# Kernel optimization log

Hardware: AMD Instinct MI355X
Metric: run time of the kernel (lower is better)

## Reference

```python
import jax, jax.numpy as jnp
import numpy as np

# ---- architecture constants (from init_kwargs) ----
BIG_K, SMALL_K = 51, 5
C_OUT, GROUP_IN = 96, 4
NK = -(-BIG_K // SMALL_K)          # 11 small kernels tile the big kernel
C_IN = C_OUT * NK                  # 1056
PADDING = SMALL_K - 1              # 4
EXTRA_PAD = PADDING - SMALL_K // 2 # 2
MID = BIG_K // 2                   # 25
REAL_PAD = [MID - i * SMALL_K - PADDING for i in range(NK)]
B, HOUT, WOUT = 8, 56, 56
HIN = HOUT + 2 * EXTRA_PAD         # 60


def setup_inputs() -> dict:
    key = jax.random.key(0)
    k1, k2, k3, k4 = jax.random.split(key, 4)
    rng = np.random.default_rng(0)
    rp = np.asarray(REAL_PAD, dtype=np.int32)
    # pad_hv: (C_IN, 2*GROUP_IN). Columns 0..G-1 horizontal shifts, G..2G-1 vertical.
    # For each (output-channel block, column) the nk channels get a random permutation of REAL_PAD.
    pad_hv = np.empty((C_IN, 2 * GROUP_IN), dtype=np.int32)
    for g in range(2 * GROUP_IN):
        for co in range(C_OUT):
            pad_hv[co * NK:(co + 1) * NK, g] = rng.permutation(rp)
    # idx_identit: (C_OUT, GROUP_IN); one randomly chosen channel inside each block.
    idx_identit = (rng.integers(0, NK, size=(C_OUT, GROUP_IN)) + np.arange(C_OUT)[:, None] * NK).astype(np.int32)
    x = jax.random.normal(k1, (B, C_IN, HIN, HIN), dtype=jnp.float32)
    w1 = jax.random.uniform(k2, (C_IN * GROUP_IN,), dtype=jnp.float32)
    w2 = jax.random.uniform(k3, (C_IN * GROUP_IN,), dtype=jnp.float32)
    w3 = jax.random.uniform(k4, (C_OUT * GROUP_IN,), dtype=jnp.float32)
    return {
        'x': x, 'w1': w1, 'w2': w2, 'w3': w3,
        'pad_hv': jnp.asarray(pad_hv), 'idx_identit': jnp.asarray(idx_identit),
        'b': B, 'hout': HOUT, 'wout': WOUT,
    }


def _forward(x, w1, w2, w3, pad_hv, idx_identit, hout, wout):
    Bx, C, H_in, W_in = x.shape
    c_out, G = idx_identit.shape
    nk = C // c_out
    ep = (H_in - hout) // 2  # extra_pad
    w1r = w1.reshape(G, C)
    w2r = w2.reshape(G, C)
    w3r = w3.reshape(G, c_out)

    # ---- horizontal shift branch (weights w1) ----
    xh = x[:, :, ep:ep + hout, :]                       # (B,C,hout,W_in)
    wpos = jnp.arange(wout)
    acc_h = jnp.zeros((Bx, C, hout, wout), x.dtype)
    for g in range(G):  # small fixed hyperparameter loop
        idxW = wpos[None, :] + ep + pad_hv[:, g][:, None]       # (C,wout)
        valid = (idxW >= 0) & (idxW < W_in)
        gat = jnp.take_along_axis(xh, jnp.clip(idxW, 0, W_in - 1)[None, :, None, :], axis=3)
        gat = jnp.where(valid[None, :, None, :], gat, 0.0)
        acc_h = acc_h + gat * w1r[g][None, :, None, None]
    out_h = acc_h.reshape(Bx, c_out, nk, hout, wout).sum(axis=2)  # scatter by idx_out (block structure)

    # ---- vertical shift branch (weights w2) ----
    xv = x[:, :, :, ep:ep + wout]                       # (B,C,H_in,wout)
    hpos = jnp.arange(hout)
    acc_v = jnp.zeros((Bx, C, hout, wout), x.dtype)
    for g in range(G):
        idxH = hpos[None, :] + ep + pad_hv[:, G + g][:, None]   # (C,hout)
        valid = (idxH >= 0) & (idxH < H_in)
        gat = jnp.take_along_axis(xv, jnp.clip(idxH, 0, H_in - 1)[None, :, :, None], axis=2)
        gat = jnp.where(valid[None, :, :, None], gat, 0.0)
        acc_v = acc_v + gat * w2r[g][None, :, None, None]
    out_v = acc_v.reshape(Bx, c_out, nk, hout, wout).sum(axis=2)

    # ---- identity branch (weights w3): pick one channel per output per group ----
    xc = x[:, :, ep:ep + hout, ep:ep + wout]            # (B,C,hout,wout)
    out_i = jnp.zeros((Bx, c_out, hout, wout), x.dtype)
    for g in range(G):
        out_i = out_i + xc[:, idx_identit[:, g]] * w3r[g][None, :, None, None]
    return out_h, out_v, out_i


def reference(x, w1, w2, w3, pad_hv, idx_identit, b, hout, wout):
    # Matches AddShift_mp_linear_module.forward: returns the three chunks (x, y, z)
    return _forward(x, w1, w2, w3, pad_hv, idx_identit, hout, wout)
```

## Files before the change

kernel.cpp:

```cpp
#include <hip/hip_runtime.h>

#define BATCH   8
#define C_OUT_N 96
#define NK      11
#define C_IN_N  1056
#define GRP     4
#define HOUT    56
#define WOUT    56
#define HIN     60
#define WIN     60
#define EP      2

#define RPAD    27
#define CPADL   28
#define STRIDE  108
#define RTOT    106
#define TILE_DW (RTOT * STRIDE)

__global__ __launch_bounds__(256, 3) void addshift_kernel(
    const float* __restrict__ x,
    const float* __restrict__ w1,
    const float* __restrict__ w2,
    const float* __restrict__ w3,
    const int*   __restrict__ pad_hv,
    const int*   __restrict__ idx_identit,
    float* __restrict__ out)
{
    const int co = blockIdx.x;
    const int b  = blockIdx.y;
    const int tid = threadIdx.x;

    __shared__ __align__(16) float tile[TILE_DW];

    {
        const float4 z4 = {0.f, 0.f, 0.f, 0.f};
        for (int j = tid; j < TILE_DW / 4; j += 256)
            ((float4*)tile)[j] = z4;
    }

    const int h0 = (tid >> 6) * 14;
    const int w  = tid & 63;
    const int wc = (w < WOUT) ? w : (WOUT - 1);

    int   kI[GRP];
    float w3v[GRP];
#pragma unroll
    for (int g = 0; g < GRP; ++g) {
        kI[g]  = idx_identit[co * GRP + g] - co * NK;
        w3v[g] = w3[g * C_OUT_N + co];
    }

    float accH[14], accV[14], accI[14];
#pragma unroll
    for (int i = 0; i < 14; ++i) { accH[i] = 0.f; accV[i] = 0.f; accI[i] = 0.f; }

    const float* chan_base = x + ((size_t)b * C_IN_N + (size_t)co * NK) * (HIN * WIN);

    float4 pre[4];
    {
        const float4* src4 = (const float4*)chan_base;
#pragma unroll
        for (int t = 0; t < 4; ++t) {
            int j = tid + t * 256;
            pre[t] = src4[j < 900 ? j : 899];
        }
    }

    __syncthreads();

    const int rowH = (h0 + EP + RPAD) * STRIDE;
    const int colV = wc + EP + CPADL;

#pragma unroll 1
    for (int k = 0; k < NK; ++k) {
#pragma unroll
        for (int t = 0; t < 4; ++t) {
            int j = tid + t * 256;
            if (j < 900) {
                int row = j / 15;
                int c4  = j - row * 15;
                *(float4*)&tile[(row + RPAD) * STRIDE + CPADL + c4 * 4] = pre[t];
            }
        }
        __syncthreads();

        if (k < NK - 1) {
            const float4* src4 = (const float4*)(chan_base + (size_t)(k + 1) * (HIN * WIN));
#pragma unroll
            for (int t = 0; t < 4; ++t) {
                int j = tid + t * 256;
                pre[t] = src4[j < 900 ? j : 899];
            }
        }

        const int c = co * NK + k;
        int ph[GRP], pv[GRP];
        float a1[GRP], a2[GRP];
#pragma unroll
        for (int g = 0; g < GRP; ++g) {
            ph[g] = pad_hv[c * 8 + g];
            pv[g] = pad_hv[c * 8 + 4 + g];
            a1[g] = w1[g * C_IN_N + c];
            a2[g] = w2[g * C_IN_N + c];
        }
        float wi = 0.f;
#pragma unroll
        for (int g = 0; g < GRP; ++g)
            if (kI[g] == k) wi += w3v[g];

#pragma unroll
        for (int g = 0; g < GRP; ++g) {
            const int offH = rowH + colV + ph[g];
            const int offV = (h0 + EP + pv[g] + RPAD) * STRIDE + colV;
#pragma unroll
            for (int i = 0; i < 14; ++i) {
                accH[i] = fmaf(tile[offH + i * STRIDE], a1[g], accH[i]);
                accV[i] = fmaf(tile[offV + i * STRIDE], a2[g], accV[i]);
            }
        }
        if (wi != 0.f) {
            const int offI = rowH + colV;
#pragma unroll
            for (int i = 0; i < 14; ++i)
                accI[i] = fmaf(tile[offI + i * STRIDE], wi, accI[i]);
        }
        __syncthreads();
    }

    if (w < WOUT) {
        const size_t OSZ = (size_t)BATCH * C_OUT_N * HOUT * WOUT;
        const size_t base = (((size_t)b * C_OUT_N + co) * HOUT + h0) * WOUT + w;
#pragma unroll
        for (int i = 0; i < 14; ++i) {
            out[base + (size_t)i * WOUT]            = accH[i];
            out[OSZ + base + (size_t)i * WOUT]      = accV[i];
            out[2 * OSZ + base + (size_t)i * WOUT]  = accI[i];
        }
    }
}

extern "C" void kernel_launch(void* const* d_in, const int* in_sizes, int n_in,
                              void* d_out, int out_size, void* d_ws, size_t ws_size,
                              hipStream_t stream) {
    const float* x   = (const float*)d_in[0];
    const float* w1  = (const float*)d_in[1];
    const float* w2  = (const float*)d_in[2];
    const float* w3  = (const float*)d_in[3];
    const int* pad_hv      = (const int*)d_in[4];
    const int* idx_identit = (const int*)d_in[5];
    float* out = (float*)d_out;

    dim3 grid(C_OUT_N, BATCH);
    dim3 block(256);
    addshift_kernel<<<grid, block, 0, stream>>>(x, w1, w2, w3, pad_hv, idx_identit, out);
}
```

Before: 239.8 us.

## Double-buffer compact LDS tiles and double the block size to 512 threads

```diff
diff --git a/kernel.cpp b/kernel.cpp
--- a/kernel.cpp
+++ b/kernel.cpp
@@ -11,13 +11,13 @@
 #define WIN     60
 #define EP      2
 
-#define RPAD    27
-#define CPADL   28
-#define STRIDE  108
-#define RTOT    106
-#define TILE_DW (RTOT * STRIDE)
+#define TS      64
+#define TROWS   60
+#define TILE_DW (TROWS * TS)
 
-__global__ __launch_bounds__(256, 3) void addshift_kernel(
+#define ROWS_PW 7
+
+__global__ __launch_bounds__(512, 6) void addshift_kernel(
     const float* __restrict__ x,
     const float* __restrict__ w1,
     const float* __restrict__ w2,
@@ -26,21 +26,16 @@
     const int*   __restrict__ idx_identit,
     float* __restrict__ out)
 {
-    const int co = blockIdx.x;
-    const int b  = blockIdx.y;
+    const int co  = blockIdx.x;
+    const int b   = blockIdx.y;
     const int tid = threadIdx.x;
 
-    __shared__ __align__(16) float tile[TILE_DW];
+    __shared__ __align__(16) float buf[2][TILE_DW];
 
-    {
-        const float4 z4 = {0.f, 0.f, 0.f, 0.f};
-        for (int j = tid; j < TILE_DW / 4; j += 256)
-            ((float4*)tile)[j] = z4;
-    }
-
-    const int h0 = (tid >> 6) * 14;
-    const int w  = tid & 63;
-    const int wc = (w < WOUT) ? w : (WOUT - 1);
+    const int wave = tid >> 6;
+    const int w    = tid & 63;
+    const int wc   = (w < WOUT) ? w : (WOUT - 1);
+    const int h0   = wave * ROWS_PW;
 
     int   kI[GRP];
     float w3v[GRP];
@@ -50,48 +45,39 @@
         w3v[g] = w3[g * C_OUT_N + co];
     }
 
-    float accH[14], accV[14], accI[14];
+    float accH[ROWS_PW], accV[ROWS_PW], accI[ROWS_PW];
 #pragma unroll
-    for (int i = 0; i < 14; ++i) { accH[i] = 0.f; accV[i] = 0.f; accI[i] = 0.f; }
+    for (int i = 0; i < ROWS_PW; ++i) { accH[i] = 0.f; accV[i] = 0.f; accI[i] = 0.f; }
 
     const float* chan_base = x + ((size_t)b * C_IN_N + (size_t)co * NK) * (HIN * WIN);
 
-    float4 pre[4];
+    float4 pre[2];
+
     {
         const float4* src4 = (const float4*)chan_base;
-#pragma unroll
-        for (int t = 0; t < 4; ++t) {
-            int j = tid + t * 256;
-            pre[t] = src4[j < 900 ? j : 899];
+        pre[0] = src4[tid];
+        int j1 = tid + 512;
+        pre[1] = src4[j1 < 900 ? j1 : 899];
+
+        {
+            int row = tid / 15, c4 = tid - row * 15;
+            *(float4*)&buf[0][row * TS + c4 * 4] = pre[0];
+            if (j1 < 900) {
+                int r1 = j1 / 15, c1 = j1 - r1 * 15;
+                *(float4*)&buf[0][r1 * TS + c1 * 4] = pre[1];
+            }
         }
+        const float4* s1 = (const float4*)(chan_base + (size_t)(HIN * WIN));
+        pre[0] = s1[tid];
+        pre[1] = s1[(tid + 512) < 900 ? (tid + 512) : 899];
     }
-
     __syncthreads();
 
-    const int rowH = (h0 + EP + RPAD) * STRIDE;
-    const int colV = wc + EP + CPADL;
+    const int cV = wc + EP;
 
 #pragma unroll 1
     for (int k = 0; k < NK; ++k) {
-#pragma unroll
-        for (int t = 0; t < 4; ++t) {
-            int j = tid + t * 256;
-            if (j < 900) {
-                int row = j / 15;
-                int c4  = j - row * 15;
-                *(float4*)&tile[(row + RPAD) * STRIDE + CPADL + c4 * 4] = pre[t];
-            }
-        }
-        __syncthreads();
-
-        if (k < NK - 1) {
-            const float4* src4 = (const float4*)(chan_base + (size_t)(k + 1) * (HIN * WIN));
-#pragma unroll
-            for (int t = 0; t < 4; ++t) {
-                int j = tid + t * 256;
-                pre[t] = src4[j < 900 ? j : 899];
-            }
-        }
+        const float* __restrict__ bf = buf[k & 1];
 
         const int c = co * NK + k;
         int ph[GRP], pv[GRP];
@@ -110,31 +96,60 @@
 
 #pragma unroll
         for (int g = 0; g < GRP; ++g) {
-            const int offH = rowH + colV + ph[g];
-            const int offV = (h0 + EP + pv[g] + RPAD) * STRIDE + colV;
+            int ix  = wc + EP + ph[g];
+            float wh = ((unsigned)ix < (unsigned)WIN) ? a1[g] : 0.f;
+            int ixc = ix < 0 ? 0 : (ix > WIN - 1 ? WIN - 1 : ix);
 #pragma unroll
-            for (int i = 0; i < 14; ++i) {
-                accH[i] = fmaf(tile[offH + i * STRIDE], a1[g], accH[i]);
-                accV[i] = fmaf(tile[offV + i * STRIDE], a2[g], accV[i]);
+            for (int i = 0; i < ROWS_PW; ++i)
+                accH[i] = fmaf(bf[(h0 + i + EP) * TS + ixc], wh, accH[i]);
+        }
+
+#pragma unroll
+        for (int g = 0; g < GRP; ++g) {
+            const int rb = h0 + EP + pv[g];
+#pragma unroll
+            for (int i = 0; i < ROWS_PW; ++i) {
+                int r   = rb + i;
+                float wv = ((unsigned)r < (unsigned)HIN) ? a2[g] : 0.f;
+                int rc  = r < 0 ? 0 : (r > HIN - 1 ? HIN - 1 : r);
+                accV[i] = fmaf(bf[rc * TS + cV], wv, accV[i]);
             }
         }
+
         if (wi != 0.f) {
-            const int offI = rowH + colV;
 #pragma unroll
-            for (int i = 0; i < 14; ++i)
-                accI[i] = fmaf(tile[offI + i * STRIDE], wi, accI[i]);
+            for (int i = 0; i < ROWS_PW; ++i)
+                accI[i] = fmaf(bf[(h0 + i + EP) * TS + cV], wi, accI[i]);
+        }
+
+        if (k < NK - 1) {
+            float* __restrict__ nb = buf[(k + 1) & 1];
+            {
+                int row = tid / 15, c4 = tid - row * 15;
+                *(float4*)&nb[row * TS + c4 * 4] = pre[0];
+                int j1 = tid + 512;
+                if (j1 < 900) {
+                    int r1 = j1 / 15, c1 = j1 - r1 * 15;
+                    *(float4*)&nb[r1 * TS + c1 * 4] = pre[1];
+                }
+            }
+            if (k < NK - 2) {
+                const float4* sn = (const float4*)(chan_base + (size_t)(k + 2) * (HIN * WIN));
+                pre[0] = sn[tid];
+                pre[1] = sn[(tid + 512) < 900 ? (tid + 512) : 899];
+            }
         }
         __syncthreads();
     }
 
     if (w < WOUT) {
-        const size_t OSZ = (size_t)BATCH * C_OUT_N * HOUT * WOUT;
+        const size_t OSZ  = (size_t)BATCH * C_OUT_N * HOUT * WOUT;
         const size_t base = (((size_t)b * C_OUT_N + co) * HOUT + h0) * WOUT + w;
 #pragma unroll
-        for (int i = 0; i < 14; ++i) {
-            out[base + (size_t)i * WOUT]            = accH[i];
-            out[OSZ + base + (size_t)i * WOUT]      = accV[i];
-            out[2 * OSZ + base + (size_t)i * WOUT]  = accI[i];
+        for (int i = 0; i < ROWS_PW; ++i) {
+            out[base + (size_t)i * WOUT]           = accH[i];
+            out[OSZ + base + (size_t)i * WOUT]     = accV[i];
+            out[2 * OSZ + base + (size_t)i * WOUT] = accI[i];
         }
     }
 }
@@ -151,6 +166,6 @@
     float* out = (float*)d_out;
 
     dim3 grid(C_OUT_N, BATCH);
-    dim3 block(256);
+    dim3 block(512);
     addshift_kernel<<<grid, block, 0, stream>>>(x, w1, w2, w3, pad_hv, idx_identit, out);
 }
```

Measured after the change: 491.9 us. 105% more time.
